# Optimization experiments

Hardware: AMD Instinct MI355X
Metric: run time of the kernel (lower is better)

Reference implementation:

```python
import jax, jax.numpy as jnp
import numpy as np

BATCH, T, N_INP, N_HID = 32, 512, 128, 1024
DT = 0.042
RHO = 0.99
INPUT_SCALING = 1.0
THRESHOLD = 0.5
RESET = 0.0
R_ = 1.0   # resistance
C_ = 1.0   # capacity
P = 0.5
HARMONIC = N_HID * P          # scalar, as in source: n_hid * p
SPIKING = N_HID - HARMONIC    # scalar, as in source


def setup_inputs() -> dict:
    key = jax.random.key(0)
    k1, k2, k3, k4, k5 = jax.random.split(key, 5)
    x = jax.random.normal(k1, (BATCH, T, N_INP), dtype=jnp.float32)
    # input-to-hidden in (0, input_scaling), per torch.rand * input_scaling
    x2h = jax.random.uniform(k2, (N_INP, N_HID), dtype=jnp.float32) * INPUT_SCALING
    # hidden-to-hidden: full topology, rescaled to spectral radius rho
    W = np.asarray(jax.random.uniform(k3, (N_HID, N_HID), minval=-1.0, maxval=1.0))
    sr = float(np.max(np.abs(np.linalg.eigvals(W))))
    h2h = jnp.asarray(W * (RHO / sr), dtype=jnp.float32)
    # gamma/epsilon sampled per-unit from uniform ranges (tuple branch of __init__)
    gamma = jax.random.uniform(k4, (N_HID,), minval=0.5, maxval=1.5, dtype=jnp.float32)
    epsilon = jax.random.uniform(k5, (N_HID,), minval=0.001, maxval=0.01, dtype=jnp.float32)
    bias = jnp.zeros((N_HID,), dtype=jnp.float32)
    return {"x": x, "x2h": x2h, "h2h": h2h, "gamma": gamma, "epsilon": epsilon, "bias": bias}


def reference(x, x2h, h2h, gamma, epsilon, bias):
    B = x.shape[0]
    dtype = x.dtype
    u_decay = 1.0 - R_ * C_ * DT  # u = u + R*C*dt*(-u)

    def step(carry, xt):
        hy, hz, u = carry
        # spiking_osc: threshold, reset, leak
        spike = (u > THRESHOLD).astype(dtype)
        u = jnp.where(spike == 1.0, RESET, u)
        u = u * u_decay
        # coupled-oscillator update
        drive = jnp.tanh(xt @ x2h + hy @ h2h + bias)
        hz = hz + DT * (drive - gamma * hy - (epsilon * (hz * HARMONIC) + u * SPIKING))
        hy = hy + DT * hz
        return (hy, hz, u), (hy, hz, u, spike)

    zeros = jnp.zeros((B, N_HID), dtype=dtype)
    (_, _, _), (hy_t, hz_t, u_t, spk_t) = jax.lax.scan(
        step, (zeros, zeros, zeros), jnp.swapaxes(x, 0, 1)
    )
    # (T, B, H) -> (B, T, H), matching the per-step lists of the original
    tr = lambda a: jnp.swapaxes(a, 0, 1)
    return tr(hy_t), tr(hz_t), tr(u_t), tr(spk_t)
```

## Files before the change

kernel.cpp:

```cpp
#include <hip/hip_runtime.h>
#include <cmath>

constexpr int  Bn  = 32, Tn = 512, NIn = 128, Hn = 1024;
constexpr long long TH  = (long long)Tn * Hn;
constexpr long long BTH = (long long)Bn * TH;
constexpr float DTc  = 0.042f;
constexpr float UDEC = 1.0f - 1.0f * 1.0f * DTc;
constexpr float HARM = 512.0f;
constexpr float SPIK = 512.0f;

__device__ unsigned g_tag[4 * 64 * 16];

__global__ void init_tag() {
    int i = threadIdx.x;
    __hip_atomic_store(&g_tag[i * 16], 0u,
                       __ATOMIC_RELAXED, __HIP_MEMORY_SCOPE_AGENT);
}

__global__ __launch_bounds__(256) void pre_gemm(const float* __restrict__ x,
                                                const float* __restrict__ x2h,
                                                const float* __restrict__ bias,
                                                float* __restrict__ pre) {
    __shared__ float xs[64 * 128];
    __shared__ float ws[128 * 64];
    const int tid = threadIdx.x;
    const int rb  = blockIdx.y * 64;
    const int cb  = blockIdx.x * 64;

#pragma unroll
    for (int i = 0; i < 8; ++i) {
        int idx = i * 1024 + tid * 4;
        int r = idx >> 7, k = idx & 127;
        *(float4*)(&xs[r * 128 + k]) =
            *(const float4*)(&x[(long long)(rb + r) * NIn + k]);
    }
#pragma unroll
    for (int i = 0; i < 8; ++i) {
        int idx = i * 1024 + tid * 4;
        int k = idx >> 6, c = idx & 63;
        *(float4*)(&ws[k * 64 + c]) =
            *(const float4*)(&x2h[(long long)k * Hn + cb + c]);
    }
    __syncthreads();

    const int tx = tid & 15, ty = tid >> 4;
    const int r0 = ty * 4, c0 = tx * 4;
    float acc[4][4] = {};
#pragma unroll 4
    for (int k = 0; k < 128; ++k) {
        float4 bv = *(const float4*)(&ws[k * 64 + c0]);
        float a0 = xs[(r0 + 0) * 128 + k];
        float a1 = xs[(r0 + 1) * 128 + k];
        float a2 = xs[(r0 + 2) * 128 + k];
        float a3 = xs[(r0 + 3) * 128 + k];
        acc[0][0] += a0 * bv.x; acc[0][1] += a0 * bv.y; acc[0][2] += a0 * bv.z; acc[0][3] += a0 * bv.w;
        acc[1][0] += a1 * bv.x; acc[1][1] += a1 * bv.y; acc[1][2] += a1 * bv.z; acc[1][3] += a1 * bv.w;
        acc[2][0] += a2 * bv.x; acc[2][1] += a2 * bv.y; acc[2][2] += a2 * bv.z; acc[2][3] += a2 * bv.w;
        acc[3][0] += a3 * bv.x; acc[3][1] += a3 * bv.y; acc[3][2] += a3 * bv.z; acc[3][3] += a3 * bv.w;
    }
    float4 bb = *(const float4*)(&bias[cb + c0]);
#pragma unroll
    for (int i = 0; i < 4; ++i) {
        float4 o;
        o.x = acc[i][0] + bb.x; o.y = acc[i][1] + bb.y;
        o.z = acc[i][2] + bb.z; o.w = acc[i][3] + bb.w;
        *(float4*)(&pre[(long long)(rb + r0 + i) * Hn + cb + c0]) = o;
    }
}

__global__ __launch_bounds__(256, 1) void ron_loop(const float* __restrict__ h2h,
                                                   const float* __restrict__ gam,
                                                   const float* __restrict__ eps,
                                                   float* __restrict__ out) {
    extern __shared__ float sm[];
    float* hyl  = sm;
    float* wt   = sm + 8 * 1028;
    float* part = wt;

    const int tid = threadIdx.x;
    const int bx  = blockIdx.x;
    const int hg  = bx & 63;
    const int bg  = bx >> 6;
    const int c0  = hg * 16;
    const int b0  = bg * 8;
    unsigned* mytag   = &g_tag[(bg * 64 + hg) * 16];
    unsigned* tagbase = &g_tag[bg * 64 * 16];

    float* hy_o = out;
    float* hz_o = out + BTH;
    float* u_o  = out + 2 * BTH;
    float* sp_o = out + 3 * BTH;

    for (int idx = tid; idx < 16 * 1024; idx += 256) {
        int cc2 = idx & 15, k = idx >> 4;
        wt[cc2 * 1028 + k] = h2h[(long long)k * Hn + c0 + cc2];
    }
    __syncthreads();

    const int ks   = tid & 31;
    const int tile = tid >> 5;
    const int tb   = tile >> 2;
    const int tc   = tile & 3;

    float4 W[4][8];
#pragma unroll
    for (int j = 0; j < 4; ++j)
#pragma unroll
        for (int m = 0; m < 8; ++m)
            W[j][m] = *(const float4*)(wt + (tc * 4 + j) * 1028 + (ks + 32 * m) * 4);

    const float* hp0 = hyl + (tb * 4 + 0) * 1028 + ks * 4;
    const float* hp1 = hp0 + 1028;
    const float* hp2 = hp0 + 2 * 1028;
    const float* hp3 = hp0 + 3 * 1028;
    float* pw = part + (tb * 64 + tc * 4) * 33 + ks;

    const int r  = tid & 127;
    const int cc = r & 15;
    const int bb = r >> 4;
    const int b  = b0 + bb;
    const int h  = c0 + cc;
    const float g = gam[h];
    const float e = eps[h];
    float hy = 0.0f, hz = 0.0f, u = 0.0f;

#define D4(dst, hv, wv)                                         \
    dst = fmaf(hv.x, wv.x, dst); dst = fmaf(hv.y, wv.y, dst);   \
    dst = fmaf(hv.z, wv.z, dst); dst = fmaf(hv.w, wv.w, dst)

    for (int t = 0; t < Tn; ++t) {
        float pre_v = 0.0f;
        if (tid < 128)
            pre_v = u_o[(long long)b * TH + (long long)t * Hn + h];

        float acc = 0.0f;
        if (t > 0) {
            const long long base = (long long)b0 * TH + (long long)(t - 1) * Hn + tid;
            float v[32];
#pragma unroll
            for (int i = 0; i < 32; ++i) {
                v[i] = __hip_atomic_load(
                    &hy_o[base + (long long)(i >> 2) * TH + (i & 3) * 256],
                    __ATOMIC_RELAXED, __HIP_MEMORY_SCOPE_AGENT);
            }
#pragma unroll
            for (int i = 0; i < 32; ++i)
                hyl[(i >> 2) * 1028 + (i & 3) * 256 + tid] = v[i];
            __syncthreads();

            float a00 = 0.f, a01 = 0.f, a02 = 0.f, a03 = 0.f;
            float a10 = 0.f, a11 = 0.f, a12 = 0.f, a13 = 0.f;
            float a20 = 0.f, a21 = 0.f, a22 = 0.f, a23 = 0.f;
            float a30 = 0.f, a31 = 0.f, a32 = 0.f, a33 = 0.f;
#pragma unroll
            for (int m = 0; m < 8; ++m) {
                const int o4 = m * 128;
                float4 h0 = *(const float4*)(hp0 + o4);
                float4 h1 = *(const float4*)(hp1 + o4);
                float4 h2 = *(const float4*)(hp2 + o4);
                float4 h3 = *(const float4*)(hp3 + o4);
                D4(a00, h0, W[0][m]); D4(a01, h0, W[1][m]); D4(a02, h0, W[2][m]); D4(a03, h0, W[3][m]);
                D4(a10, h1, W[0][m]); D4(a11, h1, W[1][m]); D4(a12, h1, W[2][m]); D4(a13, h1, W[3][m]);
                D4(a20, h2, W[0][m]); D4(a21, h2, W[1][m]); D4(a22, h2, W[2][m]); D4(a23, h2, W[3][m]);
                D4(a30, h3, W[0][m]); D4(a31, h3, W[1][m]); D4(a32, h3, W[2][m]); D4(a33, h3, W[3][m]);
            }

            pw[ 0 * 33] = a00; pw[ 1 * 33] = a01; pw[ 2 * 33] = a02; pw[ 3 * 33] = a03;
            pw[16 * 33] = a10; pw[17 * 33] = a11; pw[18 * 33] = a12; pw[19 * 33] = a13;
            pw[32 * 33] = a20; pw[33 * 33] = a21; pw[34 * 33] = a22; pw[35 * 33] = a23;
            pw[48 * 33] = a30; pw[49 * 33] = a31; pw[50 * 33] = a32; pw[51 * 33] = a33;
            __syncthreads();

            if (tid < 128) {
                const float* pr = part + r * 33;
                float s0 = 0.f, s1 = 0.f, s2 = 0.f, s3 = 0.f;
#pragma unroll
                for (int k = 0; k < 32; k += 4) {
                    s0 += pr[k + 0]; s1 += pr[k + 1];
                    s2 += pr[k + 2]; s3 += pr[k + 3];
                }
                acc = (s0 + s1) + (s2 + s3);
            }
        }

        if (tid < 128) {
            float spike = (u > 0.5f) ? 1.0f : 0.0f;
            u = (spike == 1.0f) ? 0.0f : u;
            u = u * UDEC;
            float drive = tanhf(acc + pre_v);
            hz = hz + DTc * (drive - g * hy - (e * (hz * HARM) + u * SPIK));
            hy = hy + DTc * hz;
            const long long o = (long long)b * TH + (long long)t * Hn + h;
            __hip_atomic_store(&hy_o[o], hy,
                               __ATOMIC_RELAXED, __HIP_MEMORY_SCOPE_AGENT);
            hz_o[o] = hz;
            u_o[o]  = u;
            sp_o[o] = spike;
        }

        if (t < Tn - 1) {
            __syncthreads();
            if (tid == 0)
                __hip_atomic_store(mytag, (unsigned)(t + 1),
                                   __ATOMIC_RELAXED, __HIP_MEMORY_SCOPE_AGENT);
            if (tid < 64) {
                const unsigned target = (unsigned)(t + 1);
                for (;;) {
                    unsigned v = __hip_atomic_load(&tagbase[tid * 16],
                                                   __ATOMIC_RELAXED,
                                                   __HIP_MEMORY_SCOPE_AGENT);
                    if (__ballot(v < target) == 0ull) break;
                    __builtin_amdgcn_s_sleep(1);
                }
            }
            __syncthreads();
        }
    }
#undef D4
}

extern "C" void kernel_launch(void* const* d_in, const int* in_sizes, int n_in,
                              void* d_out, int out_size, void* d_ws, size_t ws_size,
                              hipStream_t stream) {
    const float* x    = (const float*)d_in[0];
    const float* x2h  = (const float*)d_in[1];
    const float* h2h  = (const float*)d_in[2];
    const float* gam  = (const float*)d_in[3];
    const float* eps  = (const float*)d_in[4];
    const float* bias = (const float*)d_in[5];
    float* out = (float*)d_out;
    float* pre = out + 2 * BTH;

    init_tag<<<1, 256, 0, stream>>>();
    pre_gemm<<<dim3(16, 256), dim3(256), 0, stream>>>(x, x2h, bias, pre);

    const unsigned smem = (24 * 1028) * sizeof(float);
    (void)hipFuncSetAttribute((const void*)ron_loop,
                              hipFuncAttributeMaxDynamicSharedMemorySize,
                              (int)smem);
    void* args[] = {(void*)&h2h, (void*)&gam, (void*)&eps, (void*)&out};
    (void)hipLaunchCooperativeKernel((void*)ron_loop, dim3(256), dim3(256),
                                     args, smem, stream);
}
```

Measured before the change: 2.287 ms.

## Repartition recurrent blocks to 4 batches x 32 hidden and signal earlier

Each block now owns 4 batch rows and 32 hidden columns instead of 8 by 16, so there are 8 independent synchronization groups of 32 blocks rather than 4 groups of 64. Each block gathers half as much previous-step hy per step, and each group barrier polls fewer tags. The ready tag is now published before the hz/u/spike global stores, so those stores overlap with other blocks waiting. The trade-off is that each block holds twice as many h2h columns in shared memory, and the per-step k-reduction is laid out differently.

```diff
diff --git a/kernel.cpp b/kernel.cpp
--- a/kernel.cpp
+++ b/kernel.cpp
@@ -9,7 +9,7 @@
 constexpr float HARM = 512.0f;
 constexpr float SPIK = 512.0f;
 
-__device__ unsigned g_tag[4 * 64 * 16];
+__device__ unsigned g_tag[8 * 32 * 16];
 
 __global__ void init_tag() {
     int i = threadIdx.x;
@@ -74,50 +74,48 @@
                                                    float* __restrict__ out) {
     extern __shared__ float sm[];
     float* hyl  = sm;
-    float* wt   = sm + 8 * 1028;
+    float* wt   = sm + 4 * 1028;
     float* part = wt;
 
     const int tid = threadIdx.x;
     const int bx  = blockIdx.x;
-    const int hg  = bx & 63;
-    const int bg  = bx >> 6;
-    const int c0  = hg * 16;
-    const int b0  = bg * 8;
-    unsigned* mytag   = &g_tag[(bg * 64 + hg) * 16];
-    unsigned* tagbase = &g_tag[bg * 64 * 16];
+    const int bg  = bx & 7;
+    const int hg  = bx >> 3;
+    const int c0  = hg * 32;
+    const int b0  = bg * 4;
+    unsigned* mytag   = &g_tag[(bg * 32 + hg) * 16];
+    unsigned* tagbase = &g_tag[bg * 32 * 16];
 
     float* hy_o = out;
     float* hz_o = out + BTH;
     float* u_o  = out + 2 * BTH;
     float* sp_o = out + 3 * BTH;
 
-    for (int idx = tid; idx < 16 * 1024; idx += 256) {
-        int cc2 = idx & 15, k = idx >> 4;
+    for (int idx = tid; idx < 32 * 1024; idx += 256) {
+        int cc2 = idx & 31, k = idx >> 5;
         wt[cc2 * 1028 + k] = h2h[(long long)k * Hn + c0 + cc2];
     }
     __syncthreads();
 
     const int ks   = tid & 31;
     const int tile = tid >> 5;
-    const int tb   = tile >> 2;
-    const int tc   = tile & 3;
 
     float4 W[4][8];
 #pragma unroll
     for (int j = 0; j < 4; ++j)
 #pragma unroll
         for (int m = 0; m < 8; ++m)
-            W[j][m] = *(const float4*)(wt + (tc * 4 + j) * 1028 + (ks + 32 * m) * 4);
-
-    const float* hp0 = hyl + (tb * 4 + 0) * 1028 + ks * 4;
+            W[j][m] = *(const float4*)(wt + (tile * 4 + j) * 1028 + (ks + 32 * m) * 4);
+
+    const float* hp0 = hyl + 0 * 1028 + ks * 4;
     const float* hp1 = hp0 + 1028;
     const float* hp2 = hp0 + 2 * 1028;
     const float* hp3 = hp0 + 3 * 1028;
-    float* pw = part + (tb * 64 + tc * 4) * 33 + ks;
+    float* pw = part + (tile * 4) * 33 + ks;
 
     const int r  = tid & 127;
-    const int cc = r & 15;
-    const int bb = r >> 4;
+    const int cc = r & 31;
+    const int bb = r >> 5;
     const int b  = b0 + bb;
     const int h  = c0 + cc;
     const float g = gam[h];
@@ -136,15 +134,15 @@
         float acc = 0.0f;
         if (t > 0) {
             const long long base = (long long)b0 * TH + (long long)(t - 1) * Hn + tid;
-            float v[32];
-#pragma unroll
-            for (int i = 0; i < 32; ++i) {
+            float v[16];
+#pragma unroll
+            for (int i = 0; i < 16; ++i) {
                 v[i] = __hip_atomic_load(
                     &hy_o[base + (long long)(i >> 2) * TH + (i & 3) * 256],
                     __ATOMIC_RELAXED, __HIP_MEMORY_SCOPE_AGENT);
             }
 #pragma unroll
-            for (int i = 0; i < 32; ++i)
+            for (int i = 0; i < 16; ++i)
                 hyl[(i >> 2) * 1028 + (i & 3) * 256 + tid] = v[i];
             __syncthreads();
 
@@ -165,10 +163,14 @@
                 D4(a30, h3, W[0][m]); D4(a31, h3, W[1][m]); D4(a32, h3, W[2][m]); D4(a33, h3, W[3][m]);
             }
 
-            pw[ 0 * 33] = a00; pw[ 1 * 33] = a01; pw[ 2 * 33] = a02; pw[ 3 * 33] = a03;
-            pw[16 * 33] = a10; pw[17 * 33] = a11; pw[18 * 33] = a12; pw[19 * 33] = a13;
-            pw[32 * 33] = a20; pw[33 * 33] = a21; pw[34 * 33] = a22; pw[35 * 33] = a23;
-            pw[48 * 33] = a30; pw[49 * 33] = a31; pw[50 * 33] = a32; pw[51 * 33] = a33;
+            pw[(0 * 32 + 0) * 33] = a00; pw[(0 * 32 + 1) * 33] = a01;
+            pw[(0 * 32 + 2) * 33] = a02; pw[(0 * 32 + 3) * 33] = a03;
+            pw[(1 * 32 + 0) * 33] = a10; pw[(1 * 32 + 1) * 33] = a11;
+            pw[(1 * 32 + 2) * 33] = a12; pw[(1 * 32 + 3) * 33] = a13;
+            pw[(2 * 32 + 0) * 33] = a20; pw[(2 * 32 + 1) * 33] = a21;
+            pw[(2 * 32 + 2) * 33] = a22; pw[(2 * 32 + 3) * 33] = a23;
+            pw[(3 * 32 + 0) * 33] = a30; pw[(3 * 32 + 1) * 33] = a31;
+            pw[(3 * 32 + 2) * 33] = a32; pw[(3 * 32 + 3) * 33] = a33;
             __syncthreads();
 
             if (tid < 128) {
@@ -183,30 +185,39 @@
             }
         }
 
+        float spike = 0.0f;
+        long long o = 0;
         if (tid < 128) {
-            float spike = (u > 0.5f) ? 1.0f : 0.0f;
+            spike = (u > 0.5f) ? 1.0f : 0.0f;
             u = (spike == 1.0f) ? 0.0f : u;
             u = u * UDEC;
             float drive = tanhf(acc + pre_v);
             hz = hz + DTc * (drive - g * hy - (e * (hz * HARM) + u * SPIK));
             hy = hy + DTc * hz;
-            const long long o = (long long)b * TH + (long long)t * Hn + h;
+            o = (long long)b * TH + (long long)t * Hn + h;
             __hip_atomic_store(&hy_o[o], hy,
                                __ATOMIC_RELAXED, __HIP_MEMORY_SCOPE_AGENT);
+        }
+
+        if (t < Tn - 1) {
+            __syncthreads();
+            if (tid == 0)
+                __hip_atomic_store(mytag, (unsigned)(t + 1),
+                                   __ATOMIC_RELAXED, __HIP_MEMORY_SCOPE_AGENT);
+        }
+
+        if (tid < 128) {
             hz_o[o] = hz;
             u_o[o]  = u;
             sp_o[o] = spike;
         }
 
         if (t < Tn - 1) {
-            __syncthreads();
-            if (tid == 0)
-                __hip_atomic_store(mytag, (unsigned)(t + 1),
-                                   __ATOMIC_RELAXED, __HIP_MEMORY_SCOPE_AGENT);
             if (tid < 64) {
                 const unsigned target = (unsigned)(t + 1);
+                const int idx = tid & 31;
                 for (;;) {
-                    unsigned v = __hip_atomic_load(&tagbase[tid * 16],
+                    unsigned v = __hip_atomic_load(&tagbase[idx * 16],
                                                    __ATOMIC_RELAXED,
                                                    __HIP_MEMORY_SCOPE_AGENT);
                     if (__ballot(v < target) == 0ull) break;
@@ -234,7 +245,7 @@
     init_tag<<<1, 256, 0, stream>>>();
     pre_gemm<<<dim3(16, 256), dim3(256), 0, stream>>>(x, x2h, bias, pre);
 
-    const unsigned smem = (24 * 1028) * sizeof(float);
+    const unsigned smem = (4 * 1028 + 32 * 1028) * sizeof(float);
     (void)hipFuncSetAttribute((const void*)ron_loop,
                               hipFuncAttributeMaxDynamicSharedMemorySize,
                               (int)smem);
```

Result: faster. 1.837 ms (-19.7%).
